# Kernel tuning notes

Measured on AMD Instinct MI355X. Metric: run time of the kernel, lower is better.

## Reference

```python
import jax, jax.numpy as jnp
import numpy as np


def setup_inputs() -> dict:
    key = jax.random.key(0)
    k1, k2, k3, k4 = jax.random.split(key, 4)
    B, C, H, W = 8, 64, 64, 64
    K = C // 8
    x = jax.random.normal(k1, (B, C, H, W), dtype=jnp.float32)
    # 1x1 conv weights (no bias): stored as [out_ch, in_ch]
    Wf = jax.random.normal(k2, (K, C), dtype=jnp.float32) * 0.05
    Wg = jax.random.normal(k3, (K, C), dtype=jnp.float32) * 0.05
    Wh = jax.random.normal(k4, (C, C), dtype=jnp.float32) * 0.05
    # gamma initialized to zero in the module; use a nonzero value so the
    # attention path contributes to the output (and gradients) in testing.
    gamma = jnp.array([0.5], dtype=jnp.float32)
    return {"x": x, "Wf": Wf, "Wg": Wg, "Wh": Wh, "gamma": gamma}


def reference(x, Wf, Wg, Wh, gamma):
    B, C, H, W = x.shape
    N = H * W
    xf = x.reshape(B, C, N)                       # [B, C, N]
    f = jnp.einsum('kc,bcn->bkn', Wf, xf)         # [B, C//8, N]
    g = jnp.einsum('kc,bcn->bkn', Wg, xf)         # [B, C//8, N]
    h = jnp.einsum('oc,bcn->bon', Wh, xf)         # [B, C, N]
    # beta[b, i, j] = f[b,:,i] . g[b,:,j]  (unscaled attention logits)
    beta = jnp.einsum('bki,bkj->bij', f, g)       # [B, N, N]
    beta = jax.nn.softmax(beta, axis=-1)
    # res[b, c, i] = sum_j h[b, c, j] * beta[b, i, j]
    res = jnp.einsum('bcj,bij->bci', h, beta)     # [B, C, N]
    res = res.reshape(B, C, H, W)
    return gamma * res + x
```

## Files before the change

### kernel.cpp

```cpp
#include <hip/hip_runtime.h>

typedef float f32x4 __attribute__((ext_vector_type(4)));
typedef float f32x16 __attribute__((ext_vector_type(16)));
typedef short s16x8 __attribute__((ext_vector_type(8)));
typedef short s16x4 __attribute__((ext_vector_type(4)));
typedef unsigned short u16;

#define NB 8
#define NC 64
#define NN 4096

__device__ __forceinline__ u16 f2bf_rne(float f) {
    unsigned u = __float_as_uint(f);
    u += 0x7FFFu + ((u >> 16) & 1u);
    return (u16)(u >> 16);
}
__device__ __forceinline__ float bf2f(u16 v) {
    return __uint_as_float(((unsigned)v) << 16);
}
__device__ __forceinline__ unsigned cvt_pk_bf16(float lo, float hi) {
    unsigned r;
    asm("v_cvt_pk_bf16_f32 %0, %1, %2" : "=v"(r) : "v"(lo), "v"(hi));
    return r;
}
__device__ __forceinline__ void pl32_swap(unsigned &a, unsigned &b) {
    asm("v_permlane32_swap_b32 %0, %1" : "+v"(a), "+v"(b));
}
__device__ __forceinline__ float exp2_hw(float x) {
    return __builtin_amdgcn_exp2f(x);
}

#define Z16 ((f32x16){0.f,0.f,0.f,0.f,0.f,0.f,0.f,0.f,0.f,0.f,0.f,0.f,0.f,0.f,0.f,0.f})

__global__ __launch_bounds__(256, 4)
void precompute_qgh(const float* __restrict__ x,
                    const float* __restrict__ Wf,
                    const float* __restrict__ Wg,
                    const float* __restrict__ Wh,
                    u16* __restrict__ Qw, u16* __restrict__ Gw,
                    u16* __restrict__ Hf)
{
    const int b  = blockIdx.x;
    const int n0 = blockIdx.y * 64;
    const int t  = threadIdx.x;
    const int wave = t >> 6, lane = t & 63, col = lane & 15, quad = lane >> 4;
    const float* xb = x + (size_t)b * NC * NN;

    __shared__ __align__(16) u16 WL[80][72];
    __shared__ __align__(16) u16 XT[64][72];

    #pragma unroll
    for (int r5 = 0; r5 < 5; r5++) {
        int v = r5 * 256 + t;
        int m = v >> 4, ks = (v & 15) << 2;
        const float* src = (m < 64) ? (Wh + m * 64 + ks)
                         : (m < 72) ? (Wf + (m - 64) * 64 + ks)
                                    : (Wg + (m - 72) * 64 + ks);
        const float scl = (m >= 64 && m < 72) ? 1.44269504088896f : 1.0f;
        f32x4 wv = *(const f32x4*)src;
        *(unsigned*)&WL[m][ks]     = (unsigned)f2bf_rne(wv[0] * scl) | ((unsigned)f2bf_rne(wv[1] * scl) << 16);
        *(unsigned*)&WL[m][ks + 2] = (unsigned)f2bf_rne(wv[2] * scl) | ((unsigned)f2bf_rne(wv[3] * scl) << 16);
    }
    #pragma unroll
    for (int r4 = 0; r4 < 4; r4++) {
        int v = r4 * 256 + t;
        int c = v >> 4, ns = (v & 15) << 2;
        f32x4 xv = *(const f32x4*)(xb + (size_t)c * NN + n0 + ns);
        #pragma unroll
        for (int e = 0; e < 4; e++) XT[ns + e][c] = f2bf_rne(xv[e]);
    }
    __syncthreads();

    const int n = n0 + wave * 16 + col;
    s16x8 bfrag[2], afrag[5][2];
    #pragma unroll
    for (int s = 0; s < 2; s++)
        bfrag[s] = *(const s16x8*)&XT[wave * 16 + col][s * 32 + quad * 8];
    #pragma unroll
    for (int mt = 0; mt < 5; mt++)
        #pragma unroll
        for (int s = 0; s < 2; s++)
            afrag[mt][s] = *(const s16x8*)&WL[mt * 16 + col][s * 32 + quad * 8];

    f32x4 d[5];
    #pragma unroll
    for (int mt = 0; mt < 5; mt++) d[mt] = (f32x4){0.f, 0.f, 0.f, 0.f};
    #pragma unroll
    for (int s = 0; s < 2; s++)
        #pragma unroll
        for (int mt = 0; mt < 5; mt++)
            d[mt] = __builtin_amdgcn_mfma_f32_16x16x32_bf16(afrag[mt][s], bfrag[s], d[mt], 0, 0, 0);

    union { s16x4 v; u16 e[4]; } pk4;
    #pragma unroll
    for (int r = 0; r < 4; r++) pk4.e[r] = f2bf_rne(d[4][r]);
    u16* qgbase = (quad < 2 ? Qw : Gw) + ((size_t)b * NN + n) * 16;
    *(s16x4*)(qgbase + (quad & 1) * 4) = pk4.v;
    if ((quad & 1) == 0) {
        s16x8 z;
        #pragma unroll
        for (int q = 0; q < 8; q++) ((u16*)&z)[q] = 0;
        *(s16x8*)(qgbase + 8) = z;
    }

    __syncthreads();
    u16 (*Hl)[72] = WL;
    #pragma unroll
    for (int mt = 0; mt < 4; mt++)
        #pragma unroll
        for (int r = 0; r < 4; r++)
            Hl[mt * 16 + quad * 4 + r][wave * 16 + col] = f2bf_rne(d[mt][r]);
    __syncthreads();

    u16* HfB = Hf + (size_t)b * NC * NN + (size_t)blockIdx.y * 4096;
    #pragma unroll
    for (int it = 0; it < 2; it++) {
        int u = it * 256 + t;
        int s_local = u >> 7, chalf = (u >> 6) & 1, l = u & 63;
        s16x8 vv = *(const s16x8*)&Hl[chalf * 32 + (l & 31)][s_local * 16 + (l >> 5) * 8];
        *(s16x8*)(HfB + (size_t)((s_local * 2 + chalf) * 512 + l * 8)) = vv;
    }
}

__global__ __launch_bounds__(256, 4)
void attention_fused(const u16* __restrict__ Qw, const u16* __restrict__ Gw,
                     const u16* __restrict__ Hf,
                     const float* __restrict__ x, const float* __restrict__ gamma,
                     float* __restrict__ out)
{
    const int b  = blockIdx.x;
    const int i0 = blockIdx.y * 32;
    const int t  = threadIdx.x;
    const int wave = t >> 6, lane = t & 63, col = lane & 31, hi = lane >> 5;

    __shared__ __align__(16) float R0[64][36];
    __shared__ __align__(16) float R1[64][36];
    __shared__ float Ls[4][32];
    __shared__ float Sc[32];

    const u16* Qb  = Qw + (size_t)b * NN * 16;
    const u16* Gb  = Gw + (size_t)b * NN * 16;
    const u16* Hfb = Hf + (size_t)b * NC * NN;

    const float g = gamma[0];

    s16x8 qf = *(const s16x8*)(Qb + (size_t)(i0 + col) * 16 + hi * 8);

    f32x16 oacc[2];
    oacc[0] = Z16; oacc[1] = Z16;
    float ls0 = 0.f, ls1 = 0.f, ls2 = 0.f, ls3 = 0.f;

    const int jbase = wave * 1024;
    const u16* pv = Hfb + (size_t)(jbase >> 4) * 1024 + (size_t)lane * 8;

    s16x8 ga  = *(const s16x8*)(Gb + (size_t)(jbase + col) * 16 + hi * 8);
    s16x8 va0 = *(const s16x8*)(pv);
    s16x8 va1 = *(const s16x8*)(pv + 512);
    s16x8 va2 = *(const s16x8*)(pv + 1024);
    s16x8 va3 = *(const s16x8*)(pv + 1536);
    pv += 2048;

    for (int cc = 0; cc < 32; cc++) {
        s16x8 gan = *(const s16x8*)(Gb + (size_t)(jbase + cc * 32 + 32 + col) * 16 + hi * 8);
        s16x8 vn0 = *(const s16x8*)(pv);
        s16x8 vn1 = *(const s16x8*)(pv + 512);
        s16x8 vn2 = *(const s16x8*)(pv + 1024);
        s16x8 vn3 = *(const s16x8*)(pv + 1536);
        pv += 2048;

        f32x16 S = __builtin_amdgcn_mfma_f32_32x32x16_bf16(ga, qf, Z16, 0, 0, 0);
        #pragma unroll
        for (int r = 0; r < 16; r++) S[r] = exp2_hw(S[r]);
        #pragma unroll
        for (int r = 0; r < 16; r += 4) {
            ls0 += S[r]; ls1 += S[r + 1]; ls2 += S[r + 2]; ls3 += S[r + 3];
        }

        #pragma unroll
        for (int s2 = 0; s2 < 2; s2++) {
            unsigned w0 = cvt_pk_bf16(S[8*s2+0], S[8*s2+1]);
            unsigned w2 = cvt_pk_bf16(S[8*s2+4], S[8*s2+5]);
            unsigned w1 = cvt_pk_bf16(S[8*s2+2], S[8*s2+3]);
            unsigned w3 = cvt_pk_bf16(S[8*s2+6], S[8*s2+7]);
            pl32_swap(w0, w2);
            pl32_swap(w1, w3);
            union { s16x8 v; unsigned u[4]; } pb;
            pb.u[0] = w0; pb.u[1] = w1; pb.u[2] = w2; pb.u[3] = w3;
            oacc[0] = __builtin_amdgcn_mfma_f32_32x32x16_bf16(pb.v, s2 ? va2 : va0, oacc[0], 0, 0, 0);
            oacc[1] = __builtin_amdgcn_mfma_f32_32x32x16_bf16(pb.v, s2 ? va3 : va1, oacc[1], 0, 0, 0);
        }
        ga = gan; va0 = vn0; va1 = vn1; va2 = vn2; va3 = vn3;
    }

    float lsum = (ls0 + ls1) + (ls2 + ls3);
    {
        unsigned a = __float_as_uint(lsum), c2 = a;
        pl32_swap(a, c2);
        lsum = __uint_as_float(a) + __uint_as_float(c2);
    }

    if (hi == 0) Ls[wave][col] = lsum;
    if (wave & 1) {
        float (*R)[36] = (wave == 1) ? R0 : R1;
        #pragma unroll
        for (int ch = 0; ch < 2; ch++)
            #pragma unroll
            for (int r = 0; r < 16; r++)
                R[ch * 32 + col][(r & 3) + 8 * (r >> 2) + 4 * hi] = oacc[ch][r];
    }
    __syncthreads();
    if (!(wave & 1)) {
        float (*R)[36] = (wave == 0) ? R0 : R1;
        #pragma unroll
        for (int ch = 0; ch < 2; ch++)
            #pragma unroll
            for (int r = 0; r < 16; r++)
                oacc[ch][r] += R[ch * 32 + col][(r & 3) + 8 * (r >> 2) + 4 * hi];
    }
    if (wave == 1 && hi == 0)
        Sc[col] = g / (Ls[0][col] + Ls[1][col] + Ls[2][col] + Ls[3][col]);
    if (wave == 2) {
        #pragma unroll
        for (int ch = 0; ch < 2; ch++)
            #pragma unroll
            for (int r = 0; r < 16; r++)
                R1[ch * 32 + col][(r & 3) + 8 * (r >> 2) + 4 * hi] = oacc[ch][r];
    }
    __syncthreads();
    if (wave == 0) {
        #pragma unroll
        for (int ch = 0; ch < 2; ch++)
            #pragma unroll
            for (int r = 0; r < 16; r++) {
                int ii = (r & 3) + 8 * (r >> 2) + 4 * hi;
                R0[ch * 32 + col][ii] = oacc[ch][r] + R1[ch * 32 + col][ii];
            }
    }
    __syncthreads();

    const int oc = t >> 2, q4 = t & 3;
    f32x4 o0 = *(const f32x4*)&R0[oc][q4 * 8];
    f32x4 o1 = *(const f32x4*)&R0[oc][q4 * 8 + 4];
    const float* xr = x   + ((size_t)b * NC + oc) * NN + i0 + q4 * 8;
    float*    orow  = out + ((size_t)b * NC + oc) * NN + i0 + q4 * 8;
    f32x4 x0 = *(const f32x4*)(xr);
    f32x4 x1 = *(const f32x4*)(xr + 4);
    f32x4 r0, r1;
    #pragma unroll
    for (int e = 0; e < 4; e++) {
        r0[e] = o0[e] * Sc[q4 * 8 + e]     + x0[e];
        r1[e] = o1[e] * Sc[q4 * 8 + 4 + e] + x1[e];
    }
    *(f32x4*)(orow)     = r0;
    *(f32x4*)(orow + 4) = r1;
}

extern "C" void kernel_launch(void* const* d_in, const int* in_sizes, int n_in,
                              void* d_out, int out_size, void* d_ws, size_t ws_size,
                              hipStream_t stream) {
    const float* x     = (const float*)d_in[0];
    const float* Wf    = (const float*)d_in[1];
    const float* Wg    = (const float*)d_in[2];
    const float* Wh    = (const float*)d_in[3];
    const float* gamma = (const float*)d_in[4];
    float* out = (float*)d_out;

    u16* Hf = (u16*)d_ws;
    u16* Gw = Hf + (size_t)NB * NC * NN;
    u16* Qw = Gw + (size_t)NB * NN * 16;

    precompute_qgh<<<dim3(NB, 64), 256, 0, stream>>>(x, Wf, Wg, Wh, Qw, Gw, Hf);
    attention_fused<<<dim3(NB, 128), 256, 0, stream>>>(Qw, Gw, Hf, x, gamma, out);
}
```

Baseline: 105.2 us.

## Process 64 query rows per block to reuse K/V loads across two tiles

Each attention block now handles 64 query positions instead of 32, computing two score tiles per key chunk while sharing the G and H fragment loads between them. The intent is to halve global/L2 traffic for keys and values per unit of work and raise the MFMA-to-load ratio. In exchange the grid is halved to 512 blocks, register pressure roughly doubles for the accumulators (launch bounds lowered to 2 blocks per CU), and LDS use for the cross-wave reduction doubles, which reduces occupancy.

```diff
diff --git a/kernel.cpp b/kernel.cpp
--- a/kernel.cpp
+++ b/kernel.cpp
@@ -122,21 +122,23 @@
     }
 }
 
-__global__ __launch_bounds__(256, 4)
+__global__ __launch_bounds__(256, 2)
 void attention_fused(const u16* __restrict__ Qw, const u16* __restrict__ Gw,
                      const u16* __restrict__ Hf,
                      const float* __restrict__ x, const float* __restrict__ gamma,
                      float* __restrict__ out)
 {
     const int b  = blockIdx.x;
-    const int i0 = blockIdx.y * 32;
+    const int i0 = blockIdx.y * 64;
     const int t  = threadIdx.x;
     const int wave = t >> 6, lane = t & 63, col = lane & 31, hi = lane >> 5;
 
-    __shared__ __align__(16) float R0[64][36];
-    __shared__ __align__(16) float R1[64][36];
-    __shared__ float Ls[4][32];
-    __shared__ float Sc[32];
+    __shared__ __align__(16) float R0a[64][36];
+    __shared__ __align__(16) float R1a[64][36];
+    __shared__ __align__(16) float R0b[64][36];
+    __shared__ __align__(16) float R1b[64][36];
+    __shared__ float Ls[2][4][32];
+    __shared__ float Sc[2][32];
 
     const u16* Qb  = Qw + (size_t)b * NN * 16;
     const u16* Gb  = Gw + (size_t)b * NN * 16;
@@ -144,11 +146,12 @@
 
     const float g = gamma[0];
 
-    s16x8 qf = *(const s16x8*)(Qb + (size_t)(i0 + col) * 16 + hi * 8);
-
-    f32x16 oacc[2];
-    oacc[0] = Z16; oacc[1] = Z16;
-    float ls0 = 0.f, ls1 = 0.f, ls2 = 0.f, ls3 = 0.f;
+    s16x8 qf0 = *(const s16x8*)(Qb + (size_t)(i0 + col) * 16 + hi * 8);
+    s16x8 qf1 = *(const s16x8*)(Qb + (size_t)(i0 + 32 + col) * 16 + hi * 8);
+
+    f32x16 oacc[2][2];
+    oacc[0][0] = Z16; oacc[0][1] = Z16; oacc[1][0] = Z16; oacc[1][1] = Z16;
+    float ls0a = 0.f, ls0b = 0.f, ls1a = 0.f, ls1b = 0.f;
 
     const int jbase = wave * 1024;
     const u16* pv = Hfb + (size_t)(jbase >> 4) * 1024 + (size_t)lane * 8;
@@ -168,91 +171,124 @@
         s16x8 vn3 = *(const s16x8*)(pv + 1536);
         pv += 2048;
 
-        f32x16 S = __builtin_amdgcn_mfma_f32_32x32x16_bf16(ga, qf, Z16, 0, 0, 0);
-        #pragma unroll
-        for (int r = 0; r < 16; r++) S[r] = exp2_hw(S[r]);
-        #pragma unroll
-        for (int r = 0; r < 16; r += 4) {
-            ls0 += S[r]; ls1 += S[r + 1]; ls2 += S[r + 2]; ls3 += S[r + 3];
+        f32x16 S0 = __builtin_amdgcn_mfma_f32_32x32x16_bf16(ga, qf0, Z16, 0, 0, 0);
+        f32x16 S1 = __builtin_amdgcn_mfma_f32_32x32x16_bf16(ga, qf1, Z16, 0, 0, 0);
+        #pragma unroll
+        for (int r = 0; r < 16; r++) S0[r] = exp2_hw(S0[r]);
+        #pragma unroll
+        for (int r = 0; r < 16; r++) S1[r] = exp2_hw(S1[r]);
+        #pragma unroll
+        for (int r = 0; r < 16; r += 2) {
+            ls0a += S0[r]; ls0b += S0[r + 1];
+            ls1a += S1[r]; ls1b += S1[r + 1];
         }
 
         #pragma unroll
         for (int s2 = 0; s2 < 2; s2++) {
-            unsigned w0 = cvt_pk_bf16(S[8*s2+0], S[8*s2+1]);
-            unsigned w2 = cvt_pk_bf16(S[8*s2+4], S[8*s2+5]);
-            unsigned w1 = cvt_pk_bf16(S[8*s2+2], S[8*s2+3]);
-            unsigned w3 = cvt_pk_bf16(S[8*s2+6], S[8*s2+7]);
-            pl32_swap(w0, w2);
-            pl32_swap(w1, w3);
-            union { s16x8 v; unsigned u[4]; } pb;
-            pb.u[0] = w0; pb.u[1] = w1; pb.u[2] = w2; pb.u[3] = w3;
-            oacc[0] = __builtin_amdgcn_mfma_f32_32x32x16_bf16(pb.v, s2 ? va2 : va0, oacc[0], 0, 0, 0);
-            oacc[1] = __builtin_amdgcn_mfma_f32_32x32x16_bf16(pb.v, s2 ? va3 : va1, oacc[1], 0, 0, 0);
+            unsigned a0 = cvt_pk_bf16(S0[8*s2+0], S0[8*s2+1]);
+            unsigned a2 = cvt_pk_bf16(S0[8*s2+4], S0[8*s2+5]);
+            unsigned a1 = cvt_pk_bf16(S0[8*s2+2], S0[8*s2+3]);
+            unsigned a3 = cvt_pk_bf16(S0[8*s2+6], S0[8*s2+7]);
+            pl32_swap(a0, a2);
+            pl32_swap(a1, a3);
+            union { s16x8 v; unsigned u[4]; } p0;
+            p0.u[0] = a0; p0.u[1] = a1; p0.u[2] = a2; p0.u[3] = a3;
+            unsigned b0 = cvt_pk_bf16(S1[8*s2+0], S1[8*s2+1]);
+            unsigned b2 = cvt_pk_bf16(S1[8*s2+4], S1[8*s2+5]);
+            unsigned b1 = cvt_pk_bf16(S1[8*s2+2], S1[8*s2+3]);
+            unsigned b3 = cvt_pk_bf16(S1[8*s2+6], S1[8*s2+7]);
+            pl32_swap(b0, b2);
+            pl32_swap(b1, b3);
+            union { s16x8 v; unsigned u[4]; } p1;
+            p1.u[0] = b0; p1.u[1] = b1; p1.u[2] = b2; p1.u[3] = b3;
+            oacc[0][0] = __builtin_amdgcn_mfma_f32_32x32x16_bf16(p0.v, s2 ? va2 : va0, oacc[0][0], 0, 0, 0);
+            oacc[0][1] = __builtin_amdgcn_mfma_f32_32x32x16_bf16(p0.v, s2 ? va3 : va1, oacc[0][1], 0, 0, 0);
+            oacc[1][0] = __builtin_amdgcn_mfma_f32_32x32x16_bf16(p1.v, s2 ? va2 : va0, oacc[1][0], 0, 0, 0);
+            oacc[1][1] = __builtin_amdgcn_mfma_f32_32x32x16_bf16(p1.v, s2 ? va3 : va1, oacc[1][1], 0, 0, 0);
         }
         ga = gan; va0 = vn0; va1 = vn1; va2 = vn2; va3 = vn3;
     }
 
-    float lsum = (ls0 + ls1) + (ls2 + ls3);
+    float lsum0 = ls0a + ls0b;
+    float lsum1 = ls1a + ls1b;
     {
-        unsigned a = __float_as_uint(lsum), c2 = a;
+        unsigned a = __float_as_uint(lsum0), c2 = a;
         pl32_swap(a, c2);
-        lsum = __uint_as_float(a) + __uint_as_float(c2);
-    }
-
-    if (hi == 0) Ls[wave][col] = lsum;
+        lsum0 = __uint_as_float(a) + __uint_as_float(c2);
+        unsigned d = __float_as_uint(lsum1), e2 = d;
+        pl32_swap(d, e2);
+        lsum1 = __uint_as_float(d) + __uint_as_float(e2);
+    }
+
+    if (hi == 0) { Ls[0][wave][col] = lsum0; Ls[1][wave][col] = lsum1; }
     if (wave & 1) {
-        float (*R)[36] = (wave == 1) ? R0 : R1;
-        #pragma unroll
-        for (int ch = 0; ch < 2; ch++)
-            #pragma unroll
-            for (int r = 0; r < 16; r++)
-                R[ch * 32 + col][(r & 3) + 8 * (r >> 2) + 4 * hi] = oacc[ch][r];
-    }
-    __syncthreads();
-    if (!(wave & 1)) {
-        float (*R)[36] = (wave == 0) ? R0 : R1;
-        #pragma unroll
-        for (int ch = 0; ch < 2; ch++)
-            #pragma unroll
-            for (int r = 0; r < 16; r++)
-                oacc[ch][r] += R[ch * 32 + col][(r & 3) + 8 * (r >> 2) + 4 * hi];
-    }
-    if (wave == 1 && hi == 0)
-        Sc[col] = g / (Ls[0][col] + Ls[1][col] + Ls[2][col] + Ls[3][col]);
-    if (wave == 2) {
-        #pragma unroll
-        for (int ch = 0; ch < 2; ch++)
-            #pragma unroll
-            for (int r = 0; r < 16; r++)
-                R1[ch * 32 + col][(r & 3) + 8 * (r >> 2) + 4 * hi] = oacc[ch][r];
-    }
-    __syncthreads();
-    if (wave == 0) {
+        float (*Ra)[36] = (wave == 1) ? R0a : R1a;
+        float (*Rb)[36] = (wave == 1) ? R0b : R1b;
         #pragma unroll
         for (int ch = 0; ch < 2; ch++)
             #pragma unroll
             for (int r = 0; r < 16; r++) {
                 int ii = (r & 3) + 8 * (r >> 2) + 4 * hi;
-                R0[ch * 32 + col][ii] = oacc[ch][r] + R1[ch * 32 + col][ii];
+                Ra[ch * 32 + col][ii] = oacc[0][ch][r];
+                Rb[ch * 32 + col][ii] = oacc[1][ch][r];
             }
     }
     __syncthreads();
-
-    const int oc = t >> 2, q4 = t & 3;
-    f32x4 o0 = *(const f32x4*)&R0[oc][q4 * 8];
-    f32x4 o1 = *(const f32x4*)&R0[oc][q4 * 8 + 4];
-    const float* xr = x   + ((size_t)b * NC + oc) * NN + i0 + q4 * 8;
-    float*    orow  = out + ((size_t)b * NC + oc) * NN + i0 + q4 * 8;
-    f32x4 x0 = *(const f32x4*)(xr);
-    f32x4 x1 = *(const f32x4*)(xr + 4);
-    f32x4 r0, r1;
+    if (!(wave & 1)) {
+        float (*Ra)[36] = (wave == 0) ? R0a : R1a;
+        float (*Rb)[36] = (wave == 0) ? R0b : R1b;
+        #pragma unroll
+        for (int ch = 0; ch < 2; ch++)
+            #pragma unroll
+            for (int r = 0; r < 16; r++) {
+                int ii = (r & 3) + 8 * (r >> 2) + 4 * hi;
+                oacc[0][ch][r] += Ra[ch * 32 + col][ii];
+                oacc[1][ch][r] += Rb[ch * 32 + col][ii];
+            }
+    }
+    if (wave == 1 && hi == 0)
+        Sc[0][col] = g / (Ls[0][0][col] + Ls[0][1][col] + Ls[0][2][col] + Ls[0][3][col]);
+    if (wave == 3 && hi == 0)
+        Sc[1][col] = g / (Ls[1][0][col] + Ls[1][1][col] + Ls[1][2][col] + Ls[1][3][col]);
+    if (wave == 2) {
+        #pragma unroll
+        for (int ch = 0; ch < 2; ch++)
+            #pragma unroll
+            for (int r = 0; r < 16; r++) {
+                int ii = (r & 3) + 8 * (r >> 2) + 4 * hi;
+                R1a[ch * 32 + col][ii] = oacc[0][ch][r];
+                R1b[ch * 32 + col][ii] = oacc[1][ch][r];
+            }
+    }
+    __syncthreads();
+    if (wave == 0) {
+        #pragma unroll
+        for (int ch = 0; ch < 2; ch++)
+            #pragma unroll
+            for (int r = 0; r < 16; r++) {
+                int ii = (r & 3) + 8 * (r >> 2) + 4 * hi;
+                R0a[ch * 32 + col][ii] = oacc[0][ch][r] + R1a[ch * 32 + col][ii];
+                R0b[ch * 32 + col][ii] = oacc[1][ch][r] + R1b[ch * 32 + col][ii];
+            }
+    }
+    __syncthreads();
+
+    const int oc = t >> 2, q = t & 3;
+    float (*slab)[36] = (q < 2) ? R0a : R0b;
+    const float* sc = Sc[q >> 1];
+    const float* xr = x   + ((size_t)b * NC + oc) * NN + i0;
+    float*    orow  = out + ((size_t)b * NC + oc) * NN + i0;
     #pragma unroll
     for (int e = 0; e < 4; e++) {
-        r0[e] = o0[e] * Sc[q4 * 8 + e]     + x0[e];
-        r1[e] = o1[e] * Sc[q4 * 8 + 4 + e] + x1[e];
-    }
-    *(f32x4*)(orow)     = r0;
-    *(f32x4*)(orow + 4) = r1;
+        const int il = q * 16 + e * 4;
+        const int ii = (q & 1) * 16 + e * 4;
+        f32x4 o = *(const f32x4*)&slab[oc][ii];
+        f32x4 xv = *(const f32x4*)(xr + il);
+        f32x4 rv;
+        #pragma unroll
+        for (int k = 0; k < 4; k++) rv[k] = o[k] * sc[ii + k] + xv[k];
+        *(f32x4*)(orow + il) = rv;
+    }
 }
 
 extern "C" void kernel_launch(void* const* d_in, const int* in_sizes, int n_in,
@@ -270,5 +306,5 @@
     u16* Qw = Gw + (size_t)NB * NN * 16;
 
     precompute_qgh<<<dim3(NB, 64), 256, 0, stream>>>(x, Wf, Wg, Wh, Qw, Gw, Hf);
-    attention_fused<<<dim3(NB, 128), 256, 0, stream>>>(Qw, Gw, Hf, x, gamma, out);
-}
+    attention_fused<<<dim3(NB, 64), 256, 0, stream>>>(Qw, Gw, Hf, x, gamma, out);
+}
```

Result: faster. 99.37 us (-5.5%).

## Widen attention tile to 128 queries per block with 8 waves sharing K/V loads

Applied to the files above, without the earlier changes.

Each block now covers 128 query rows with 512 threads. Every wave handles two 32-row query tiles against its quarter of the key range, so each G/H fragment loaded from global memory feeds twice as many MFMAs, cutting K/V traffic per unit of compute. The key loop is double-buffered two chunks ahead and raises wave priority around the MFMA/exp section. The cross-wave reduction and output write are reworked into two passes through a larger shared slab, which adds more barriers and more register pressure, and the grid shrinks to 256 blocks.

```diff
diff --git a/kernel.cpp b/kernel.cpp
--- a/kernel.cpp
+++ b/kernel.cpp
@@ -99,7 +99,7 @@
     if ((quad & 1) == 0) {
         s16x8 z;
         #pragma unroll
-        for (int q = 0; q < 8; q++) ((u16*)&z)[q] = 0;
+        for (int qz = 0; qz < 8; qz++) ((u16*)&z)[qz] = 0;
         *(s16x8*)(qgbase + 8) = z;
     }
 
@@ -122,137 +122,207 @@
     }
 }
 
-__global__ __launch_bounds__(256, 4)
+__global__ __launch_bounds__(512, 2)
 void attention_fused(const u16* __restrict__ Qw, const u16* __restrict__ Gw,
                      const u16* __restrict__ Hf,
                      const float* __restrict__ x, const float* __restrict__ gamma,
                      float* __restrict__ out)
 {
     const int b  = blockIdx.x;
-    const int i0 = blockIdx.y * 32;
+    const int i0 = blockIdx.y * 128;
     const int t  = threadIdx.x;
     const int wave = t >> 6, lane = t & 63, col = lane & 31, hi = lane >> 5;
-
-    __shared__ __align__(16) float R0[64][36];
-    __shared__ __align__(16) float R1[64][36];
-    __shared__ float Ls[4][32];
-    __shared__ float Sc[32];
+    const int q = wave >> 1, sown = wave & 1;
+
+    __shared__ __align__(16) float Slab[2][64][72];
+    __shared__ float Lsh[4][4][32];
+    __shared__ float Sc4[4][32];
 
     const u16* Qb  = Qw + (size_t)b * NN * 16;
     const u16* Gb  = Gw + (size_t)b * NN * 16;
     const u16* Hfb = Hf + (size_t)b * NC * NN;
-
     const float g = gamma[0];
 
-    s16x8 qf = *(const s16x8*)(Qb + (size_t)(i0 + col) * 16 + hi * 8);
-
-    f32x16 oacc[2];
-    oacc[0] = Z16; oacc[1] = Z16;
-    float ls0 = 0.f, ls1 = 0.f, ls2 = 0.f, ls3 = 0.f;
-
-    const int jbase = wave * 1024;
-    const u16* pv = Hfb + (size_t)(jbase >> 4) * 1024 + (size_t)lane * 8;
-
-    s16x8 ga  = *(const s16x8*)(Gb + (size_t)(jbase + col) * 16 + hi * 8);
-    s16x8 va0 = *(const s16x8*)(pv);
-    s16x8 va1 = *(const s16x8*)(pv + 512);
-    s16x8 va2 = *(const s16x8*)(pv + 1024);
-    s16x8 va3 = *(const s16x8*)(pv + 1536);
-    pv += 2048;
-
-    for (int cc = 0; cc < 32; cc++) {
-        s16x8 gan = *(const s16x8*)(Gb + (size_t)(jbase + cc * 32 + 32 + col) * 16 + hi * 8);
-        s16x8 vn0 = *(const s16x8*)(pv);
-        s16x8 vn1 = *(const s16x8*)(pv + 512);
-        s16x8 vn2 = *(const s16x8*)(pv + 1024);
-        s16x8 vn3 = *(const s16x8*)(pv + 1536);
-        pv += 2048;
-
-        f32x16 S = __builtin_amdgcn_mfma_f32_32x32x16_bf16(ga, qf, Z16, 0, 0, 0);
-        #pragma unroll
-        for (int r = 0; r < 16; r++) S[r] = exp2_hw(S[r]);
-        #pragma unroll
-        for (int r = 0; r < 16; r += 4) {
-            ls0 += S[r]; ls1 += S[r + 1]; ls2 += S[r + 2]; ls3 += S[r + 3];
-        }
-
-        #pragma unroll
-        for (int s2 = 0; s2 < 2; s2++) {
-            unsigned w0 = cvt_pk_bf16(S[8*s2+0], S[8*s2+1]);
-            unsigned w2 = cvt_pk_bf16(S[8*s2+4], S[8*s2+5]);
-            unsigned w1 = cvt_pk_bf16(S[8*s2+2], S[8*s2+3]);
-            unsigned w3 = cvt_pk_bf16(S[8*s2+6], S[8*s2+7]);
-            pl32_swap(w0, w2);
-            pl32_swap(w1, w3);
-            union { s16x8 v; unsigned u[4]; } pb;
-            pb.u[0] = w0; pb.u[1] = w1; pb.u[2] = w2; pb.u[3] = w3;
-            oacc[0] = __builtin_amdgcn_mfma_f32_32x32x16_bf16(pb.v, s2 ? va2 : va0, oacc[0], 0, 0, 0);
-            oacc[1] = __builtin_amdgcn_mfma_f32_32x32x16_bf16(pb.v, s2 ? va3 : va1, oacc[1], 0, 0, 0);
-        }
-        ga = gan; va0 = vn0; va1 = vn1; va2 = vn2; va3 = vn3;
-    }
-
-    float lsum = (ls0 + ls1) + (ls2 + ls3);
+    const int ibase = i0 + sown * 64;
+    s16x8 qf0 = *(const s16x8*)(Qb + (size_t)(ibase + col) * 16 + hi * 8);
+    s16x8 qf1 = *(const s16x8*)(Qb + (size_t)(ibase + 32 + col) * 16 + hi * 8);
+
+    f32x16 o00 = Z16, o01 = Z16, o10 = Z16, o11 = Z16;
+    float ls0a = 0.f, ls0b = 0.f, ls1a = 0.f, ls1b = 0.f;
+
+    const int jbase = q * 1024;
+    const u16* pvb = Hfb + (size_t)(jbase >> 4) * 1024 + (size_t)lane * 8;
+    const u16* gb0 = Gb + (size_t)(jbase + col) * 16 + hi * 8;
+
+#define LOADC(GA,V0,V1,V2,V3,c) do {                                  \
+    GA = *(const s16x8*)(gb0 + (size_t)(c) * 512);                    \
+    const u16* _p = pvb + (size_t)(c) * 2048;                         \
+    V0 = *(const s16x8*)(_p);                                         \
+    V1 = *(const s16x8*)(_p + 512);                                   \
+    V2 = *(const s16x8*)(_p + 1024);                                  \
+    V3 = *(const s16x8*)(_p + 1536); } while (0)
+
+#define COMPUTEC(GA,V0,V1,V2,V3) do {                                               \
+    __builtin_amdgcn_s_setprio(1);                                                  \
+    f32x16 S0 = __builtin_amdgcn_mfma_f32_32x32x16_bf16(GA, qf0, Z16, 0, 0, 0);     \
+    f32x16 S1 = __builtin_amdgcn_mfma_f32_32x32x16_bf16(GA, qf1, Z16, 0, 0, 0);     \
+    _Pragma("unroll") for (int r = 0; r < 16; r++) S0[r] = exp2_hw(S0[r]);          \
+    _Pragma("unroll") for (int r = 0; r < 16; r++) S1[r] = exp2_hw(S1[r]);          \
+    _Pragma("unroll") for (int r = 0; r < 16; r += 2) {                             \
+        ls0a += S0[r]; ls0b += S0[r + 1];                                           \
+        ls1a += S1[r]; ls1b += S1[r + 1]; }                                         \
+    _Pragma("unroll") for (int s2 = 0; s2 < 2; s2++) {                              \
+        unsigned a0 = cvt_pk_bf16(S0[8*s2+0], S0[8*s2+1]);                          \
+        unsigned a2 = cvt_pk_bf16(S0[8*s2+4], S0[8*s2+5]);                          \
+        unsigned a1 = cvt_pk_bf16(S0[8*s2+2], S0[8*s2+3]);                          \
+        unsigned a3 = cvt_pk_bf16(S0[8*s2+6], S0[8*s2+7]);                          \
+        pl32_swap(a0, a2); pl32_swap(a1, a3);                                       \
+        union { s16x8 v; unsigned u[4]; } p0;                                       \
+        p0.u[0] = a0; p0.u[1] = a1; p0.u[2] = a2; p0.u[3] = a3;                     \
+        unsigned b0 = cvt_pk_bf16(S1[8*s2+0], S1[8*s2+1]);                          \
+        unsigned b2 = cvt_pk_bf16(S1[8*s2+4], S1[8*s2+5]);                          \
+        unsigned b1 = cvt_pk_bf16(S1[8*s2+2], S1[8*s2+3]);                          \
+        unsigned b3 = cvt_pk_bf16(S1[8*s2+6], S1[8*s2+7]);                          \
+        pl32_swap(b0, b2); pl32_swap(b1, b3);                                       \
+        union { s16x8 v; unsigned u[4]; } p1;                                       \
+        p1.u[0] = b0; p1.u[1] = b1; p1.u[2] = b2; p1.u[3] = b3;                     \
+        o00 = __builtin_amdgcn_mfma_f32_32x32x16_bf16(p0.v, s2 ? V2 : V0, o00, 0, 0, 0); \
+        o01 = __builtin_amdgcn_mfma_f32_32x32x16_bf16(p0.v, s2 ? V3 : V1, o01, 0, 0, 0); \
+        o10 = __builtin_amdgcn_mfma_f32_32x32x16_bf16(p1.v, s2 ? V2 : V0, o10, 0, 0, 0); \
+        o11 = __builtin_amdgcn_mfma_f32_32x32x16_bf16(p1.v, s2 ? V3 : V1, o11, 0, 0, 0); \
+    }                                                                               \
+    __builtin_amdgcn_s_setprio(0); } while (0)
+
+    s16x8 gA, vA0, vA1, vA2, vA3;
+    s16x8 gB, vB0, vB1, vB2, vB3;
+    s16x8 gC, vC0, vC1, vC2, vC3;
+    LOADC(gA, vA0, vA1, vA2, vA3, 0);
+    LOADC(gB, vB0, vB1, vB2, vB3, 1);
+
+    for (int it = 0; it < 16; it++) {
+        LOADC(gC, vC0, vC1, vC2, vC3, 2 * it + 2);
+        COMPUTEC(gA, vA0, vA1, vA2, vA3);
+        gA = gC; vA0 = vC0; vA1 = vC1; vA2 = vC2; vA3 = vC3;
+        LOADC(gC, vC0, vC1, vC2, vC3, 2 * it + 3);
+        COMPUTEC(gB, vB0, vB1, vB2, vB3);
+        gB = gC; vB0 = vC0; vB1 = vC1; vB2 = vC2; vB3 = vC3;
+    }
+
+    float lsum0 = ls0a + ls0b;
+    float lsum1 = ls1a + ls1b;
     {
-        unsigned a = __float_as_uint(lsum), c2 = a;
+        unsigned a = __float_as_uint(lsum0), c2 = a;
         pl32_swap(a, c2);
-        lsum = __uint_as_float(a) + __uint_as_float(c2);
-    }
-
-    if (hi == 0) Ls[wave][col] = lsum;
-    if (wave & 1) {
-        float (*R)[36] = (wave == 1) ? R0 : R1;
-        #pragma unroll
-        for (int ch = 0; ch < 2; ch++)
-            #pragma unroll
-            for (int r = 0; r < 16; r++)
-                R[ch * 32 + col][(r & 3) + 8 * (r >> 2) + 4 * hi] = oacc[ch][r];
-    }
-    __syncthreads();
-    if (!(wave & 1)) {
-        float (*R)[36] = (wave == 0) ? R0 : R1;
-        #pragma unroll
-        for (int ch = 0; ch < 2; ch++)
-            #pragma unroll
-            for (int r = 0; r < 16; r++)
-                oacc[ch][r] += R[ch * 32 + col][(r & 3) + 8 * (r >> 2) + 4 * hi];
-    }
-    if (wave == 1 && hi == 0)
-        Sc[col] = g / (Ls[0][col] + Ls[1][col] + Ls[2][col] + Ls[3][col]);
-    if (wave == 2) {
-        #pragma unroll
-        for (int ch = 0; ch < 2; ch++)
-            #pragma unroll
-            for (int r = 0; r < 16; r++)
-                R1[ch * 32 + col][(r & 3) + 8 * (r >> 2) + 4 * hi] = oacc[ch][r];
-    }
-    __syncthreads();
-    if (wave == 0) {
-        #pragma unroll
-        for (int ch = 0; ch < 2; ch++)
-            #pragma unroll
-            for (int r = 0; r < 16; r++) {
-                int ii = (r & 3) + 8 * (r >> 2) + 4 * hi;
-                R0[ch * 32 + col][ii] = oacc[ch][r] + R1[ch * 32 + col][ii];
-            }
-    }
-    __syncthreads();
-
-    const int oc = t >> 2, q4 = t & 3;
-    f32x4 o0 = *(const f32x4*)&R0[oc][q4 * 8];
-    f32x4 o1 = *(const f32x4*)&R0[oc][q4 * 8 + 4];
-    const float* xr = x   + ((size_t)b * NC + oc) * NN + i0 + q4 * 8;
-    float*    orow  = out + ((size_t)b * NC + oc) * NN + i0 + q4 * 8;
-    f32x4 x0 = *(const f32x4*)(xr);
-    f32x4 x1 = *(const f32x4*)(xr + 4);
-    f32x4 r0, r1;
-    #pragma unroll
-    for (int e = 0; e < 4; e++) {
-        r0[e] = o0[e] * Sc[q4 * 8 + e]     + x0[e];
-        r1[e] = o1[e] * Sc[q4 * 8 + 4 + e] + x1[e];
-    }
-    *(f32x4*)(orow)     = r0;
-    *(f32x4*)(orow + 4) = r1;
+        lsum0 = __uint_as_float(a) + __uint_as_float(c2);
+        unsigned d = __float_as_uint(lsum1), e2 = d;
+        pl32_swap(d, e2);
+        lsum1 = __uint_as_float(d) + __uint_as_float(e2);
+    }
+
+    if (hi == 0) {
+        Lsh[sown * 2 + 0][q][col] = lsum0;
+        Lsh[sown * 2 + 1][q][col] = lsum1;
+    }
+
+#define II(r) (((r) & 3) + 8 * ((r) >> 2) + 4 * hi)
+    #pragma unroll
+    for (int s = 0; s < 2; s++) {
+        const bool act = (sown == s);
+        if (act && q == 1) {
+            #pragma unroll
+            for (int r = 0; r < 16; r++) {
+                int ii = II(r);
+                Slab[0][col][ii]           = o00[r];
+                Slab[0][32 + col][ii]      = o01[r];
+                Slab[0][col][32 + ii]      = o10[r];
+                Slab[0][32 + col][32 + ii] = o11[r];
+            }
+        }
+        if (act && q == 3) {
+            #pragma unroll
+            for (int r = 0; r < 16; r++) {
+                int ii = II(r);
+                Slab[1][col][ii]           = o00[r];
+                Slab[1][32 + col][ii]      = o01[r];
+                Slab[1][col][32 + ii]      = o10[r];
+                Slab[1][32 + col][32 + ii] = o11[r];
+            }
+        }
+        __syncthreads();
+        if (s == 0 && wave == 0) {
+            #pragma unroll
+            for (int T = 0; T < 4; T++)
+                Sc4[T][col] = g / (Lsh[T][0][col] + Lsh[T][1][col] +
+                                   Lsh[T][2][col] + Lsh[T][3][col]);
+        }
+        if (act && q == 0) {
+            #pragma unroll
+            for (int r = 0; r < 16; r++) {
+                int ii = II(r);
+                o00[r] += Slab[0][col][ii];
+                o01[r] += Slab[0][32 + col][ii];
+                o10[r] += Slab[0][col][32 + ii];
+                o11[r] += Slab[0][32 + col][32 + ii];
+            }
+        }
+        if (act && q == 2) {
+            #pragma unroll
+            for (int r = 0; r < 16; r++) {
+                int ii = II(r);
+                o00[r] += Slab[1][col][ii];
+                o01[r] += Slab[1][32 + col][ii];
+                o10[r] += Slab[1][col][32 + ii];
+                o11[r] += Slab[1][32 + col][32 + ii];
+            }
+            #pragma unroll
+            for (int r = 0; r < 16; r++) {
+                int ii = II(r);
+                Slab[1][col][ii]           = o00[r];
+                Slab[1][32 + col][ii]      = o01[r];
+                Slab[1][col][32 + ii]      = o10[r];
+                Slab[1][32 + col][32 + ii] = o11[r];
+            }
+        }
+        __syncthreads();
+        if (act && q == 0) {
+            #pragma unroll
+            for (int r = 0; r < 16; r++) {
+                int ii = II(r);
+                Slab[0][col][ii]           = o00[r] + Slab[1][col][ii];
+                Slab[0][32 + col][ii]      = o01[r] + Slab[1][32 + col][ii];
+                Slab[0][col][32 + ii]      = o10[r] + Slab[1][col][32 + ii];
+                Slab[0][32 + col][32 + ii] = o11[r] + Slab[1][32 + col][32 + ii];
+            }
+        }
+        __syncthreads();
+        {
+            const int oc = t >> 3, q8 = t & 7;
+            const int il = q8 * 8;
+            const int T  = s * 2 + (il >> 5);
+            const int ii0 = il & 31;
+            f32x4 sc0 = *(const f32x4*)&Sc4[T][ii0];
+            f32x4 sc1 = *(const f32x4*)&Sc4[T][ii0 + 4];
+            f32x4 o0 = *(const f32x4*)&Slab[0][oc][il];
+            f32x4 o1 = *(const f32x4*)&Slab[0][oc][il + 4];
+            const int gi = i0 + s * 64 + il;
+            const float* xr = x   + ((size_t)b * NC + oc) * NN + gi;
+            float*    orow  = out + ((size_t)b * NC + oc) * NN + gi;
+            f32x4 x0 = *(const f32x4*)(xr);
+            f32x4 x1 = *(const f32x4*)(xr + 4);
+            f32x4 r0, r1;
+            #pragma unroll
+            for (int e = 0; e < 4; e++) {
+                r0[e] = o0[e] * sc0[e] + x0[e];
+                r1[e] = o1[e] * sc1[e] + x1[e];
+            }
+            *(f32x4*)(orow)     = r0;
+            *(f32x4*)(orow + 4) = r1;
+        }
+        __syncthreads();
+    }
+#undef II
+#undef LOADC
+#undef COMPUTEC
 }
 
 extern "C" void kernel_launch(void* const* d_in, const int* in_sizes, int n_in,
@@ -270,5 +340,5 @@
     u16* Qw = Gw + (size_t)NB * NN * 16;
 
     precompute_qgh<<<dim3(NB, 64), 256, 0, stream>>>(x, Wf, Wg, Wh, Qw, Gw, Hf);
-    attention_fused<<<dim3(NB, 128), 256, 0, stream>>>(Qw, Gw, Hf, x, gamma, out);
-}
+    attention_fused<<<dim3(NB, 32), 512, 0, stream>>>(Qw, Gw, Hf, x, gamma, out);
+}
```

New measurement: 100.4 us. -4.6%, faster.

## Process 64 query rows per block with 8 waves sharing G/H loads

Applied to the files above, without the earlier changes.

Each block now covers 64 query rows using two Q fragments, and 8 waves each handle 512 keys. Every loaded G and H fragment therefore feeds twice as many MFMAs, halving global/L2 traffic for the K/V stream per output. The change also adds s_setprio around the MFMA/exp sections and moves loads to the end of the iteration. The cross-wave reduction becomes a longer tree with more barriers and LDS traffic, and register pressure rises with four accumulators.

```diff
diff --git a/kernel.cpp b/kernel.cpp
--- a/kernel.cpp
+++ b/kernel.cpp
@@ -99,7 +99,7 @@
     if ((quad & 1) == 0) {
         s16x8 z;
         #pragma unroll
-        for (int q = 0; q < 8; q++) ((u16*)&z)[q] = 0;
+        for (int qz = 0; qz < 8; qz++) ((u16*)&z)[qz] = 0;
         *(s16x8*)(qgbase + 8) = z;
     }
 
@@ -122,137 +122,192 @@
     }
 }
 
-__global__ __launch_bounds__(256, 4)
+__global__ __launch_bounds__(512, 4)
 void attention_fused(const u16* __restrict__ Qw, const u16* __restrict__ Gw,
                      const u16* __restrict__ Hf,
                      const float* __restrict__ x, const float* __restrict__ gamma,
                      float* __restrict__ out)
 {
     const int b  = blockIdx.x;
-    const int i0 = blockIdx.y * 32;
+    const int i0 = blockIdx.y * 64;
     const int t  = threadIdx.x;
     const int wave = t >> 6, lane = t & 63, col = lane & 31, hi = lane >> 5;
 
-    __shared__ __align__(16) float R0[64][36];
-    __shared__ __align__(16) float R1[64][36];
-    __shared__ float Ls[4][32];
-    __shared__ float Sc[32];
+    __shared__ __align__(16) float Slab[2][64][68];
+    __shared__ float Lsh[2][8][32];
+    __shared__ float Sc[2][32];
 
     const u16* Qb  = Qw + (size_t)b * NN * 16;
     const u16* Gb  = Gw + (size_t)b * NN * 16;
     const u16* Hfb = Hf + (size_t)b * NC * NN;
-
     const float g = gamma[0];
 
-    s16x8 qf = *(const s16x8*)(Qb + (size_t)(i0 + col) * 16 + hi * 8);
-
-    f32x16 oacc[2];
-    oacc[0] = Z16; oacc[1] = Z16;
-    float ls0 = 0.f, ls1 = 0.f, ls2 = 0.f, ls3 = 0.f;
-
-    const int jbase = wave * 1024;
-    const u16* pv = Hfb + (size_t)(jbase >> 4) * 1024 + (size_t)lane * 8;
-
-    s16x8 ga  = *(const s16x8*)(Gb + (size_t)(jbase + col) * 16 + hi * 8);
-    s16x8 va0 = *(const s16x8*)(pv);
-    s16x8 va1 = *(const s16x8*)(pv + 512);
-    s16x8 va2 = *(const s16x8*)(pv + 1024);
-    s16x8 va3 = *(const s16x8*)(pv + 1536);
-    pv += 2048;
-
-    for (int cc = 0; cc < 32; cc++) {
-        s16x8 gan = *(const s16x8*)(Gb + (size_t)(jbase + cc * 32 + 32 + col) * 16 + hi * 8);
-        s16x8 vn0 = *(const s16x8*)(pv);
-        s16x8 vn1 = *(const s16x8*)(pv + 512);
-        s16x8 vn2 = *(const s16x8*)(pv + 1024);
-        s16x8 vn3 = *(const s16x8*)(pv + 1536);
-        pv += 2048;
-
-        f32x16 S = __builtin_amdgcn_mfma_f32_32x32x16_bf16(ga, qf, Z16, 0, 0, 0);
-        #pragma unroll
-        for (int r = 0; r < 16; r++) S[r] = exp2_hw(S[r]);
-        #pragma unroll
-        for (int r = 0; r < 16; r += 4) {
-            ls0 += S[r]; ls1 += S[r + 1]; ls2 += S[r + 2]; ls3 += S[r + 3];
+    s16x8 qf0 = *(const s16x8*)(Qb + (size_t)(i0 + col) * 16 + hi * 8);
+    s16x8 qf1 = *(const s16x8*)(Qb + (size_t)(i0 + 32 + col) * 16 + hi * 8);
+
+    f32x16 o00 = Z16, o01 = Z16, o10 = Z16, o11 = Z16;
+    float ls0a = 0.f, ls0b = 0.f, ls1a = 0.f, ls1b = 0.f;
+
+    const int jbase = wave * 512;
+    const u16* pvb = Hfb + (size_t)(jbase >> 4) * 1024 + (size_t)lane * 8;
+    const u16* gb0 = Gb + (size_t)(jbase + col) * 16 + hi * 8;
+
+    s16x8 ga = *(const s16x8*)(gb0);
+    s16x8 v0 = *(const s16x8*)(pvb);
+    s16x8 v1 = *(const s16x8*)(pvb + 512);
+    s16x8 v2 = *(const s16x8*)(pvb + 1024);
+    s16x8 v3 = *(const s16x8*)(pvb + 1536);
+
+    for (int cc = 0; cc < 16; cc++) {
+        __builtin_amdgcn_s_setprio(1);
+        {
+            f32x16 S = __builtin_amdgcn_mfma_f32_32x32x16_bf16(ga, qf0, Z16, 0, 0, 0);
+            #pragma unroll
+            for (int r = 0; r < 16; r++) S[r] = exp2_hw(S[r]);
+            #pragma unroll
+            for (int r = 0; r < 16; r += 2) { ls0a += S[r]; ls0b += S[r + 1]; }
+            #pragma unroll
+            for (int s2 = 0; s2 < 2; s2++) {
+                unsigned w0 = cvt_pk_bf16(S[8*s2+0], S[8*s2+1]);
+                unsigned w2 = cvt_pk_bf16(S[8*s2+4], S[8*s2+5]);
+                unsigned w1 = cvt_pk_bf16(S[8*s2+2], S[8*s2+3]);
+                unsigned w3 = cvt_pk_bf16(S[8*s2+6], S[8*s2+7]);
+                pl32_swap(w0, w2); pl32_swap(w1, w3);
+                union { s16x8 v; unsigned u[4]; } p;
+                p.u[0] = w0; p.u[1] = w1; p.u[2] = w2; p.u[3] = w3;
+                o00 = __builtin_amdgcn_mfma_f32_32x32x16_bf16(p.v, s2 ? v2 : v0, o00, 0, 0, 0);
+                o01 = __builtin_amdgcn_mfma_f32_32x32x16_bf16(p.v, s2 ? v3 : v1, o01, 0, 0, 0);
+            }
         }
-
-        #pragma unroll
-        for (int s2 = 0; s2 < 2; s2++) {
-            unsigned w0 = cvt_pk_bf16(S[8*s2+0], S[8*s2+1]);
-            unsigned w2 = cvt_pk_bf16(S[8*s2+4], S[8*s2+5]);
-            unsigned w1 = cvt_pk_bf16(S[8*s2+2], S[8*s2+3]);
-            unsigned w3 = cvt_pk_bf16(S[8*s2+6], S[8*s2+7]);
-            pl32_swap(w0, w2);
-            pl32_swap(w1, w3);
-            union { s16x8 v; unsigned u[4]; } pb;
-            pb.u[0] = w0; pb.u[1] = w1; pb.u[2] = w2; pb.u[3] = w3;
-            oacc[0] = __builtin_amdgcn_mfma_f32_32x32x16_bf16(pb.v, s2 ? va2 : va0, oacc[0], 0, 0, 0);
-            oacc[1] = __builtin_amdgcn_mfma_f32_32x32x16_bf16(pb.v, s2 ? va3 : va1, oacc[1], 0, 0, 0);
+        {
+            f32x16 S = __builtin_amdgcn_mfma_f32_32x32x16_bf16(ga, qf1, Z16, 0, 0, 0);
+            __builtin_amdgcn_s_setprio(0);
+            ga = *(const s16x8*)(gb0 + (size_t)(cc + 1) * 512);
+            __builtin_amdgcn_s_setprio(1);
+            #pragma unroll
+            for (int r = 0; r < 16; r++) S[r] = exp2_hw(S[r]);
+            #pragma unroll
+            for (int r = 0; r < 16; r += 2) { ls1a += S[r]; ls1b += S[r + 1]; }
+            #pragma unroll
+            for (int s2 = 0; s2 < 2; s2++) {
+                unsigned w0 = cvt_pk_bf16(S[8*s2+0], S[8*s2+1]);
+                unsigned w2 = cvt_pk_bf16(S[8*s2+4], S[8*s2+5]);
+                unsigned w1 = cvt_pk_bf16(S[8*s2+2], S[8*s2+3]);
+                unsigned w3 = cvt_pk_bf16(S[8*s2+6], S[8*s2+7]);
+                pl32_swap(w0, w2); pl32_swap(w1, w3);
+                union { s16x8 v; unsigned u[4]; } p;
+                p.u[0] = w0; p.u[1] = w1; p.u[2] = w2; p.u[3] = w3;
+                o10 = __builtin_amdgcn_mfma_f32_32x32x16_bf16(p.v, s2 ? v2 : v0, o10, 0, 0, 0);
+                o11 = __builtin_amdgcn_mfma_f32_32x32x16_bf16(p.v, s2 ? v3 : v1, o11, 0, 0, 0);
+            }
         }
-        ga = gan; va0 = vn0; va1 = vn1; va2 = vn2; va3 = vn3;
-    }
-
-    float lsum = (ls0 + ls1) + (ls2 + ls3);
+        __builtin_amdgcn_s_setprio(0);
+        {
+            const u16* np = pvb + (size_t)(cc + 1) * 2048;
+            v0 = *(const s16x8*)(np);
+            v1 = *(const s16x8*)(np + 512);
+            v2 = *(const s16x8*)(np + 1024);
+            v3 = *(const s16x8*)(np + 1536);
+        }
+    }
+
+    float lsum0 = ls0a + ls0b;
+    float lsum1 = ls1a + ls1b;
     {
-        unsigned a = __float_as_uint(lsum), c2 = a;
+        unsigned a = __float_as_uint(lsum0), c2 = a;
         pl32_swap(a, c2);
-        lsum = __uint_as_float(a) + __uint_as_float(c2);
-    }
-
-    if (hi == 0) Ls[wave][col] = lsum;
-    if (wave & 1) {
-        float (*R)[36] = (wave == 1) ? R0 : R1;
-        #pragma unroll
-        for (int ch = 0; ch < 2; ch++)
-            #pragma unroll
-            for (int r = 0; r < 16; r++)
-                R[ch * 32 + col][(r & 3) + 8 * (r >> 2) + 4 * hi] = oacc[ch][r];
-    }
-    __syncthreads();
-    if (!(wave & 1)) {
-        float (*R)[36] = (wave == 0) ? R0 : R1;
-        #pragma unroll
-        for (int ch = 0; ch < 2; ch++)
-            #pragma unroll
-            for (int r = 0; r < 16; r++)
-                oacc[ch][r] += R[ch * 32 + col][(r & 3) + 8 * (r >> 2) + 4 * hi];
-    }
-    if (wave == 1 && hi == 0)
-        Sc[col] = g / (Ls[0][col] + Ls[1][col] + Ls[2][col] + Ls[3][col]);
-    if (wave == 2) {
-        #pragma unroll
-        for (int ch = 0; ch < 2; ch++)
-            #pragma unroll
-            for (int r = 0; r < 16; r++)
-                R1[ch * 32 + col][(r & 3) + 8 * (r >> 2) + 4 * hi] = oacc[ch][r];
-    }
+        lsum0 = __uint_as_float(a) + __uint_as_float(c2);
+        unsigned d = __float_as_uint(lsum1), e2 = d;
+        pl32_swap(d, e2);
+        lsum1 = __uint_as_float(d) + __uint_as_float(e2);
+    }
+    if (hi == 0) { Lsh[0][wave][col] = lsum0; Lsh[1][wave][col] = lsum1; }
+
+#define PUB(s) do {                                                        \
+    _Pragma("unroll") for (int rb = 0; rb < 4; rb++) {                     \
+        f32x4 wv;                                                          \
+        _Pragma("unroll") for (int e = 0; e < 4; e++) wv[e] = o00[rb*4+e]; \
+        *(f32x4*)&Slab[s][col][8*rb + 4*hi] = wv;                          \
+        _Pragma("unroll") for (int e = 0; e < 4; e++) wv[e] = o01[rb*4+e]; \
+        *(f32x4*)&Slab[s][32 + col][8*rb + 4*hi] = wv;                     \
+        _Pragma("unroll") for (int e = 0; e < 4; e++) wv[e] = o10[rb*4+e]; \
+        *(f32x4*)&Slab[s][col][32 + 8*rb + 4*hi] = wv;                     \
+        _Pragma("unroll") for (int e = 0; e < 4; e++) wv[e] = o11[rb*4+e]; \
+        *(f32x4*)&Slab[s][32 + col][32 + 8*rb + 4*hi] = wv;                \
+    } } while (0)
+#define ABS(s) do {                                                        \
+    _Pragma("unroll") for (int rb = 0; rb < 4; rb++) {                     \
+        f32x4 a0 = *(const f32x4*)&Slab[s][col][8*rb + 4*hi];              \
+        f32x4 a1 = *(const f32x4*)&Slab[s][32 + col][8*rb + 4*hi];         \
+        f32x4 a2 = *(const f32x4*)&Slab[s][col][32 + 8*rb + 4*hi];         \
+        f32x4 a3 = *(const f32x4*)&Slab[s][32 + col][32 + 8*rb + 4*hi];    \
+        _Pragma("unroll") for (int e = 0; e < 4; e++) {                    \
+            o00[rb*4+e] += a0[e]; o01[rb*4+e] += a1[e];                    \
+            o10[rb*4+e] += a2[e]; o11[rb*4+e] += a3[e]; }                  \
+    } } while (0)
+
+    if (wave == 1) PUB(0);
+    if (wave == 5) PUB(1);
+    __syncthreads();
+    if (wave == 0) ABS(0);
+    if (wave == 4) ABS(1);
+    if (wave == 1) {
+        Sc[hi][col] = g / (Lsh[hi][0][col] + Lsh[hi][1][col] + Lsh[hi][2][col] +
+                           Lsh[hi][3][col] + Lsh[hi][4][col] + Lsh[hi][5][col] +
+                           Lsh[hi][6][col] + Lsh[hi][7][col]);
+    }
+    __syncthreads();
+    if (wave == 3) PUB(0);
+    if (wave == 7) PUB(1);
+    __syncthreads();
+    if (wave == 2) ABS(0);
+    if (wave == 6) ABS(1);
+    __syncthreads();
+    if (wave == 2) PUB(0);
+    if (wave == 6) PUB(1);
+    __syncthreads();
+    if (wave == 0) ABS(0);
+    if (wave == 4) ABS(1);
+    __syncthreads();
+    if (wave == 4) PUB(0);
     __syncthreads();
     if (wave == 0) {
-        #pragma unroll
-        for (int ch = 0; ch < 2; ch++)
-            #pragma unroll
-            for (int r = 0; r < 16; r++) {
-                int ii = (r & 3) + 8 * (r >> 2) + 4 * hi;
-                R0[ch * 32 + col][ii] = oacc[ch][r] + R1[ch * 32 + col][ii];
-            }
-    }
-    __syncthreads();
-
-    const int oc = t >> 2, q4 = t & 3;
-    f32x4 o0 = *(const f32x4*)&R0[oc][q4 * 8];
-    f32x4 o1 = *(const f32x4*)&R0[oc][q4 * 8 + 4];
-    const float* xr = x   + ((size_t)b * NC + oc) * NN + i0 + q4 * 8;
-    float*    orow  = out + ((size_t)b * NC + oc) * NN + i0 + q4 * 8;
-    f32x4 x0 = *(const f32x4*)(xr);
-    f32x4 x1 = *(const f32x4*)(xr + 4);
-    f32x4 r0, r1;
-    #pragma unroll
-    for (int e = 0; e < 4; e++) {
-        r0[e] = o0[e] * Sc[q4 * 8 + e]     + x0[e];
-        r1[e] = o1[e] * Sc[q4 * 8 + 4 + e] + x1[e];
-    }
-    *(f32x4*)(orow)     = r0;
-    *(f32x4*)(orow + 4) = r1;
+        ABS(0);
+        #pragma unroll
+        for (int rb = 0; rb < 4; rb++) {
+            f32x4 s0 = *(const f32x4*)&Sc[0][8*rb + 4*hi];
+            f32x4 s1 = *(const f32x4*)&Sc[1][8*rb + 4*hi];
+            f32x4 wv;
+            #pragma unroll
+            for (int e = 0; e < 4; e++) wv[e] = o00[rb*4+e] * s0[e];
+            *(f32x4*)&Slab[0][col][8*rb + 4*hi] = wv;
+            #pragma unroll
+            for (int e = 0; e < 4; e++) wv[e] = o01[rb*4+e] * s0[e];
+            *(f32x4*)&Slab[0][32 + col][8*rb + 4*hi] = wv;
+            #pragma unroll
+            for (int e = 0; e < 4; e++) wv[e] = o10[rb*4+e] * s1[e];
+            *(f32x4*)&Slab[0][col][32 + 8*rb + 4*hi] = wv;
+            #pragma unroll
+            for (int e = 0; e < 4; e++) wv[e] = o11[rb*4+e] * s1[e];
+            *(f32x4*)&Slab[0][32 + col][32 + 8*rb + 4*hi] = wv;
+        }
+    }
+    __syncthreads();
+#undef PUB
+#undef ABS
+
+    {
+        const int oc = t >> 3, q8 = t & 7;
+        const int il = q8 * 8;
+        f32x4 o0 = *(const f32x4*)&Slab[0][oc][il];
+        f32x4 o1 = *(const f32x4*)&Slab[0][oc][il + 4];
+        const float* xr = x   + ((size_t)b * NC + oc) * NN + i0 + il;
+        float*    orow  = out + ((size_t)b * NC + oc) * NN + i0 + il;
+        f32x4 x0 = *(const f32x4*)(xr);
+        f32x4 x1 = *(const f32x4*)(xr + 4);
+        *(f32x4*)(orow)     = o0 + x0;
+        *(f32x4*)(orow + 4) = o1 + x1;
+    }
 }
 
 extern "C" void kernel_launch(void* const* d_in, const int* in_sizes, int n_in,
@@ -270,5 +325,5 @@
     u16* Qw = Gw + (size_t)NB * NN * 16;
 
     precompute_qgh<<<dim3(NB, 64), 256, 0, stream>>>(x, Wf, Wg, Wh, Qw, Gw, Hf);
-    attention_fused<<<dim3(NB, 128), 256, 0, stream>>>(Qw, Gw, Hf, x, gamma, out);
-}
+    attention_fused<<<dim3(NB, 64), 512, 0, stream>>>(Qw, Gw, Hf, x, gamma, out);
+}
```

After: 102.8 us. 2.3% less time.
